# Optimization experiments

Hardware: AMD Instinct MI355X
Metric: run time of the kernel (lower is better)

## Reference

```python
import jax, jax.numpy as jnp
import numpy as np

N = 1024          # nodes per atom and per input graph / barycenter
K = 8             # num_atoms
OT_LAYERS = 3     # proximal-point outer iterations inside fgwd
SINKHORN_LAYERS = 3
GWB_LAYERS = 2    # barycenter alternating-optimization iterations
PROX_BETA = 0.1   # proximal / entropic regularization strength
EPS = 1e-16


def fgwd(Gs, ps, Gb, pb):
    """Gromov-Wasserstein distance via proximal point + Sinkhorn.
    Gs:(ns,ns), ps:(ns,1), Gb:(nb,nb), pb:(nb,1). Returns (d, T) with T:(ns,nb).
    Square-loss GW cost: c(T) = f1(Gs) ps 1^T + 1 (f2(Gb) pb)^T - 2 Gs T Gb^T."""
    ns, nb = Gs.shape[0], Gb.shape[0]
    cost_st = ((Gs * Gs) @ ps) + ((Gb * Gb) @ pb).T  # (ns,1)+(1,nb) -> (ns,nb)
    T0 = ps @ pb.T  # independent-coupling init

    def ot_step(T, _):
        cost = cost_st - 2.0 * (Gs @ T @ Gb.T)
        kernel = jnp.exp(-cost / PROX_BETA) * T  # proximal-point kernel

        def sink(carry, _):
            a, b = carry
            b = pb / (kernel.T @ a + EPS)
            a = ps / (kernel @ b + EPS)
            return (a, b), None

        (a, b), _ = jax.lax.scan(sink, (ps, pb), None, length=SINKHORN_LAYERS)
        return (a * kernel) * b.T, None

    T, _ = jax.lax.scan(ot_step, T0, None, length=OT_LAYERS)
    cost = cost_st - 2.0 * (Gs @ T @ Gb.T)
    d = jnp.sum(cost * T)
    return d, T


def setup_inputs() -> dict:
    key = jax.random.key(0)
    k1, k2, k3 = jax.random.split(key, 3)
    Gm = jax.random.uniform(k1, (N, N), jnp.float32)          # input graph (sigmoid-range adjacency)
    pm = jnp.ones((N, 1), jnp.float32) / N                    # uniform node distribution
    atoms_presig = jax.random.normal(k2, (K, N, N), jnp.float32)  # pre-sigmoid atom params
    probs = jnp.ones((K, N, 1), jnp.float32) / N              # uniform atom distributions
    weights = jax.nn.softmax(jax.random.normal(k3, (K,), jnp.float32))  # output_weights
    return {"Gm": Gm, "pm": pm, "atoms_presig": atoms_presig, "probs": probs,
            "weights": weights}


def reference(Gm, pm, atoms_presig, probs, weights):
    Gk = jax.nn.sigmoid(atoms_presig)              # output_atoms: (K,N,N)
    G_bary, pb = Gm, pm                            # init_mode=0 -> barycenter init from input M
    fgwd_v = jax.vmap(fgwd, in_axes=(0, 0, None, None))
    denom = pb @ pb.T                              # pb pb^T normalizer
    for _ in range(GWB_LAYERS):
        _, trans = fgwd_v(Gk, probs, G_bary, pb)   # trans: (K,N,N)
        # comp_fgwb: sum_k w_k * T_k^T G_k T_k / (pb pb^T)
        GT = jnp.einsum('knm,kmj->knj', Gk, trans)
        G_bary = jnp.einsum('k,kni,knj->ij', weights, trans, GT) / denom
    d_fgw, _ = fgwd(Gm, pm, G_bary, pb)
    return d_fgw, G_bary
```

## Files before the change

kernel.cpp:

```cpp
#include <hip/hip_runtime.h>
#include <math.h>

#define N_   1024
#define K_   8
#define OTL  3
#define SKL  3
#define GWBL 2
#define INVB 10.0f
#define EPSV 1e-16f
#define INVN (1.0f / 1024.0f)
#define NN   ((size_t)N_ * N_)
#define KN   (K_ * N_)

typedef __attribute__((ext_vector_type(8))) short short8;
typedef __attribute__((ext_vector_type(4))) float f32x4;
typedef unsigned short bfu;

__device__ __forceinline__ float b2f(bfu u) {
    unsigned x = ((unsigned)u) << 16;
    return __builtin_bit_cast(float, x);
}
__device__ __forceinline__ bfu f2b(float f) {
    unsigned u = __builtin_bit_cast(unsigned, f);
    unsigned r = u + 0x7fffu + ((u >> 16) & 1u);
    return (bfu)(r >> 16);
}

template<int EPI>
__global__ __launch_bounds__(256, 2)
void bgemm_k(const bfu* __restrict__ A, const bfu* __restrict__ B,
             void* __restrict__ Cp, size_t sA, size_t sB, size_t sC,
             const float* __restrict__ rv, const float* __restrict__ cv,
             const float* __restrict__ wts, float* __restrict__ rs) {
    __shared__ bfu As[2][128 * 32];
    __shared__ bfu Bs[2][128 * 32];

    const int z  = blockIdx.x;
    const int bm = blockIdx.y * 128, bn = blockIdx.z * 128;
    const int tid = threadIdx.x;
    const int lane = tid & 63, wv = tid >> 6;
    const int wr = wv >> 1, wc = wv & 1;

    if (EPI == 0) {
        if (rs && blockIdx.y == 0 && blockIdx.z == 0) {
            const float4 zf = {0.f, 0.f, 0.f, 0.f};
            #pragma unroll
            for (int b = 0; b < 3; ++b)
                *(float4*)&rs[b * KN + z * N_ + tid * 4] = zf;
        }
    }

    const bfu* Az = A + (size_t)z * sA;
    const bfu* Bz = B + (size_t)z * sB;

    const int sr = tid >> 2;
    const int sk = (tid & 3) * 8;
    const int fr = lane & 15;
    const int ks = (lane >> 4) * 8;

    f32x4 acc[4][4];
    #pragma unroll
    for (int i = 0; i < 4; i++)
        #pragma unroll
        for (int j = 0; j < 4; j++) acc[i][j] = (f32x4)0.f;

    for (int k0 = 0; k0 < N_; k0 += 64) {
        __syncthreads();
        #pragma unroll
        for (int sg = 0; sg < 2; ++sg) {
            #pragma unroll
            for (int h = 0; h < 2; ++h) {
                const int row = sr + h * 64;
                const bfu* ga = Az + (size_t)(bm + row) * N_ + k0 + sg * 32 + sk;
                const bfu* gb = Bz + (size_t)(bn + row) * N_ + k0 + sg * 32 + sk;
                __builtin_amdgcn_global_load_lds(
                    (const __attribute__((address_space(1))) unsigned int*)ga,
                    (__attribute__((address_space(3))) unsigned int*)&As[sg][row * 32 + sk],
                    16, 0, 0);
                __builtin_amdgcn_global_load_lds(
                    (const __attribute__((address_space(1))) unsigned int*)gb,
                    (__attribute__((address_space(3))) unsigned int*)&Bs[sg][row * 32 + sk],
                    16, 0, 0);
            }
        }
        __syncthreads();

        #pragma unroll
        for (int sg = 0; sg < 2; ++sg) {
            short8 af[4], bf[4];
            #pragma unroll
            for (int mi = 0; mi < 4; ++mi)
                af[mi] = *(const short8*)&As[sg][(wr * 64 + mi * 16 + fr) * 32 + ks];
            #pragma unroll
            for (int ni = 0; ni < 4; ++ni)
                bf[ni] = *(const short8*)&Bs[sg][(wc * 64 + ni * 16 + fr) * 32 + ks];
            #pragma unroll
            for (int mi = 0; mi < 4; ++mi)
                #pragma unroll
                for (int ni = 0; ni < 4; ++ni)
                    acc[mi][ni] = __builtin_amdgcn_mfma_f32_16x16x32_bf16(
                        af[mi], bf[ni], acc[mi][ni], 0, 0, 0);
        }
    }

    const int r0 = bm + wr * 64, c0 = bn + wc * 64;
    const int rq = (lane >> 4) * 4;

    if (EPI == 1) {
        float* Cz = (float*)Cp + (size_t)z * sC;
        const float w = wts[z];
        #pragma unroll
        for (int mi = 0; mi < 4; ++mi)
            #pragma unroll
            for (int ni = 0; ni < 4; ++ni)
                #pragma unroll
                for (int q = 0; q < 4; ++q)
                    Cz[(size_t)(r0 + mi * 16 + rq + q) * N_ + c0 + ni * 16 + fr]
                        = w * acc[mi][ni][q];
    } else if (EPI == 0) {
        bfu* Cz = (bfu*)Cp + (size_t)z * sC;
        #pragma unroll
        for (int mi = 0; mi < 4; ++mi)
            #pragma unroll
            for (int ni = 0; ni < 4; ++ni)
                #pragma unroll
                for (int q = 0; q < 4; ++q)
                    Cz[(size_t)(r0 + mi * 16 + rq + q) * N_ + c0 + ni * 16 + fr]
                        = f2b(acc[mi][ni][q]);
    } else {
        bfu* Cz = (bfu*)Cp + (size_t)z * sC;
        const float* rvz = rv + z * N_;
        float rsum[4][4];
        #pragma unroll
        for (int mi = 0; mi < 4; ++mi)
            #pragma unroll
            for (int q = 0; q < 4; ++q) rsum[mi][q] = 0.f;
        #pragma unroll
        for (int mi = 0; mi < 4; ++mi)
            #pragma unroll
            for (int ni = 0; ni < 4; ++ni)
                #pragma unroll
                for (int q = 0; q < 4; ++q) {
                    const int row = r0 + mi * 16 + rq + q;
                    const int col = c0 + ni * 16 + fr;
                    const float cost = rvz[col] + cv[row] - 2.f * acc[mi][ni][q];
                    const float t = b2f(Cz[(size_t)row * N_ + col]);
                    const bfu tn = f2b(expf(-cost * INVB) * t);
                    Cz[(size_t)row * N_ + col] = tn;
                    rsum[mi][q] += b2f(tn);
                }
        #pragma unroll
        for (int mi = 0; mi < 4; ++mi)
            #pragma unroll
            for (int q = 0; q < 4; ++q) {
                float v = rsum[mi][q];
                v += __shfl_xor(v, 1);
                v += __shfl_xor(v, 2);
                v += __shfl_xor(v, 4);
                v += __shfl_xor(v, 8);
                if (fr == 0)
                    atomicAdd(&rs[z * N_ + r0 + mi * 16 + rq + q], v);
            }
    }
}

template<int EPI>
__global__ __launch_bounds__(256, 2)
void gemm64_k(const bfu* __restrict__ A, const bfu* __restrict__ B,
              void* __restrict__ Cp,
              const float* __restrict__ rv, const float* __restrict__ cv,
              float* __restrict__ rs, float* __restrict__ dout) {
    __shared__ bfu As[64 * 32];
    __shared__ bfu Bs[64 * 32];
    const int bn = blockIdx.x * 64;
    const int bm = blockIdx.y * 64;
    const int tid = threadIdx.x;
    const int lane = tid & 63, wv = tid >> 6;
    const int wr = wv >> 1, wc = wv & 1;
    const int sr = tid >> 2, sk = (tid & 3) * 8;
    const int fr = lane & 15, ks = (lane >> 4) * 8;

    if (EPI == 0) {
        if (blockIdx.x == 0 && blockIdx.y == 0) {
            if (rs) {
                const float4 zf = {0.f, 0.f, 0.f, 0.f};
                #pragma unroll
                for (int b = 0; b < 3; ++b)
                    *(float4*)&rs[b * KN + tid * 4] = zf;
            }
            if (dout && tid == 0) *dout = 0.f;
        }
    }

    f32x4 acc[2][2];
    #pragma unroll
    for (int i = 0; i < 2; i++)
        #pragma unroll
        for (int j = 0; j < 2; j++) acc[i][j] = (f32x4)0.f;

    for (int k0 = 0; k0 < N_; k0 += 32) {
        __syncthreads();
        __builtin_amdgcn_global_load_lds(
            (const __attribute__((address_space(1))) unsigned int*)
                (A + (size_t)(bm + sr) * N_ + k0 + sk),
            (__attribute__((address_space(3))) unsigned int*)&As[sr * 32 + sk],
            16, 0, 0);
        __builtin_amdgcn_global_load_lds(
            (const __attribute__((address_space(1))) unsigned int*)
                (B + (size_t)(bn + sr) * N_ + k0 + sk),
            (__attribute__((address_space(3))) unsigned int*)&Bs[sr * 32 + sk],
            16, 0, 0);
        __syncthreads();
        short8 af[2], bf[2];
        #pragma unroll
        for (int mi = 0; mi < 2; ++mi)
            af[mi] = *(const short8*)&As[(wr * 32 + mi * 16 + fr) * 32 + ks];
        #pragma unroll
        for (int ni = 0; ni < 2; ++ni)
            bf[ni] = *(const short8*)&Bs[(wc * 32 + ni * 16 + fr) * 32 + ks];
        #pragma unroll
        for (int mi = 0; mi < 2; ++mi)
            #pragma unroll
            for (int ni = 0; ni < 2; ++ni)
                acc[mi][ni] = __builtin_amdgcn_mfma_f32_16x16x32_bf16(
                    af[mi], bf[ni], acc[mi][ni], 0, 0, 0);
    }

    const int r0 = bm + wr * 32, c0 = bn + wc * 32;
    const int rq = (lane >> 4) * 4;

    if (EPI == 0) {
        bfu* C = (bfu*)Cp;
        #pragma unroll
        for (int mi = 0; mi < 2; ++mi)
            #pragma unroll
            for (int ni = 0; ni < 2; ++ni)
                #pragma unroll
                for (int q = 0; q < 4; ++q)
                    C[(size_t)(r0 + mi * 16 + rq + q) * N_ + c0 + ni * 16 + fr]
                        = f2b(acc[mi][ni][q]);
    } else if (EPI == 2) {
        bfu* C = (bfu*)Cp;
        float rsum[2][4];
        #pragma unroll
        for (int mi = 0; mi < 2; ++mi)
            #pragma unroll
            for (int q = 0; q < 4; ++q) rsum[mi][q] = 0.f;
        #pragma unroll
        for (int mi = 0; mi < 2; ++mi)
            #pragma unroll
            for (int ni = 0; ni < 2; ++ni)
                #pragma unroll
                for (int q = 0; q < 4; ++q) {
                    const int row = r0 + mi * 16 + rq + q;
                    const int col = c0 + ni * 16 + fr;
                    const float cost = rv[col] + cv[row] - 2.f * acc[mi][ni][q];
                    const float t = b2f(C[(size_t)row * N_ + col]);
                    const bfu tn = f2b(expf(-cost * INVB) * t);
                    C[(size_t)row * N_ + col] = tn;
                    rsum[mi][q] += b2f(tn);
                }
        #pragma unroll
        for (int mi = 0; mi < 2; ++mi)
            #pragma unroll
            for (int q = 0; q < 4; ++q) {
                float v = rsum[mi][q];
                v += __shfl_xor(v, 1);
                v += __shfl_xor(v, 2);
                v += __shfl_xor(v, 4);
                v += __shfl_xor(v, 8);
                if (fr == 0)
                    atomicAdd(&rs[r0 + mi * 16 + rq + q], v);
            }
    } else {
        const bfu* C = (const bfu*)Cp;
        float bs = 0.f;
        #pragma unroll
        for (int mi = 0; mi < 2; ++mi)
            #pragma unroll
            for (int ni = 0; ni < 2; ++ni)
                #pragma unroll
                for (int q = 0; q < 4; ++q) {
                    const int row = r0 + mi * 16 + rq + q;
                    const int col = c0 + ni * 16 + fr;
                    bs += (rv[col] + cv[row] - 2.f * acc[mi][ni][q]) *
                          b2f(C[(size_t)row * N_ + col]);
                }
        #pragma unroll
        for (int off = 32; off; off >>= 1) bs += __shfl_down(bs, off);
        __shared__ float wred[4];
        if (lane == 0) wred[wv] = bs;
        __syncthreads();
        if (tid == 0) atomicAdd(dout, wred[0] + wred[1] + wred[2] + wred[3]);
    }
}

__global__ __launch_bounds__(256)
void prox1_k(bfu* __restrict__ Tt, const float* __restrict__ c2,
             const float* __restrict__ u, const float* __restrict__ d2,
             const float* __restrict__ w, const float* __restrict__ ps,
             const float* __restrict__ pb, float* __restrict__ bv,
             float* __restrict__ rs1, int zs, int nb) {
    const int b = blockIdx.x;
    const int z  = (nb == 8) ? (b & 7) : 0;
    const int rp = (nb == 8) ? (b >> 3) : b;
    const int tid = threadIdx.x;

    if (rp < 2) {
        const float4 zf = {0.f, 0.f, 0.f, 0.f};
        *(float4*)&rs1[rp * KN + z * N_ + tid * 4] = zf;
    }

    const int half = tid >> 7;
    const int j = rp * 2 + half;
    const int i0 = (tid & 127) * 8;
    const float d2j = d2[j], wj = w[j], pbj = pb[j];
    const float* c2z = c2 + z * zs + i0;
    const float* uz  = u  + z * zs + i0;
    const float* psz = ps + z * zs + i0;
    bfu o[8];
    float s = 0.f;
    #pragma unroll
    for (int t = 0; t < 8; ++t) {
        const float cost = c2z[t] + d2j - 2.f * uz[t] * wj;
        o[t] = f2b(expf(-cost * INVB) * psz[t] * pbj);
        s += b2f(o[t]);
    }
    *(short8*)&Tt[((size_t)z << 20) + ((size_t)j << 10) + i0] = *(short8*)o;
    #pragma unroll
    for (int off = 32; off; off >>= 1) s += __shfl_down(s, off);
    __shared__ float red[4];
    if ((tid & 63) == 0) red[tid >> 6] = s;
    __syncthreads();
    if ((tid & 127) == 0)
        bv[z * N_ + j] = pbj / ((red[half * 2] + red[half * 2 + 1]) * INVN + EPSV);
}

template<int NB>
__global__ __launch_bounds__(256)
void redprox_k(const float* __restrict__ part, bfu* __restrict__ Gbt,
               float* __restrict__ d2out, float* __restrict__ wout,
               float* __restrict__ out1,
               const float* __restrict__ c2, const float* __restrict__ u,
               bfu* __restrict__ Tt, float* __restrict__ bv,
               float* __restrict__ rs12) {
    const int tid = threadIdx.x;
    if (blockIdx.x < 16) {
        const float4 zf = {0.f, 0.f, 0.f, 0.f};
        *(float4*)&rs12[blockIdx.x * 1024 + tid * 4] = zf;
    }
    __shared__ float red[8];
    __shared__ float bc[2];
    #pragma unroll
    for (int rep = 0; rep < 2; ++rep) {
        const int row = blockIdx.x + rep * 512;
        const size_t idx = (size_t)row * N_ + tid * 4;
        float4 s = *(const float4*)(part + idx);
        #pragma unroll
        for (int sl = 1; sl < K_; ++sl) {
            float4 v = *(const float4*)(part + (size_t)sl * NN + idx);
            s.x += v.x; s.y += v.y; s.z += v.z; s.w += v.w;
        }
        const float sc = 1048576.f;
        s.x *= sc; s.y *= sc; s.z *= sc; s.w *= sc;
        bfu o[4];
        o[0] = f2b(s.x); o[1] = f2b(s.y); o[2] = f2b(s.z); o[3] = f2b(s.w);
        *(ulong1*)&Gbt[idx] = *(ulong1*)o;
        if (out1) {
            out1[idx + 0] = s.x; out1[idx + 1] = s.y;
            out1[idx + 2] = s.z; out1[idx + 3] = s.w;
        }
        float r2 = s.x * s.x + s.y * s.y + s.z * s.z + s.w * s.w;
        float r1 = s.x + s.y + s.z + s.w;
        #pragma unroll
        for (int off = 32; off; off >>= 1) {
            r2 += __shfl_down(r2, off);
            r1 += __shfl_down(r1, off);
        }
        if ((tid & 63) == 0) {
            red[(tid >> 6) * 2]     = r2;
            red[(tid >> 6) * 2 + 1] = r1;
        }
        __syncthreads();
        if (tid == 0) {
            const float d2j = (red[0] + red[2] + red[4] + red[6]) * INVN;
            const float wj  = (red[1] + red[3] + red[5] + red[7]) * INVN;
            d2out[row] = d2j; wout[row] = wj;
            bc[0] = d2j; bc[1] = wj;
        }
        __syncthreads();
        const float d2j = bc[0], wj = bc[1];
        const float sc2 = INVN * INVN;
        #pragma unroll
        for (int z = 0; z < NB; ++z) {
            const float4 cv4 = *(const float4*)(c2 + z * N_ + tid * 4);
            const float4 uv4 = *(const float4*)(u  + z * N_ + tid * 4);
            bfu t[4];
            t[0] = f2b(expf(-(cv4.x + d2j - 2.f * uv4.x * wj) * INVB) * sc2);
            t[1] = f2b(expf(-(cv4.y + d2j - 2.f * uv4.y * wj) * INVB) * sc2);
            t[2] = f2b(expf(-(cv4.z + d2j - 2.f * uv4.z * wj) * INVB) * sc2);
            t[3] = f2b(expf(-(cv4.w + d2j - 2.f * uv4.w * wj) * INVB) * sc2);
            *(ulong1*)&Tt[(size_t)z * NN + idx] = *(ulong1*)t;
            float rsum = b2f(t[0]) + b2f(t[1]) + b2f(t[2]) + b2f(t[3]);
            #pragma unroll
            for (int off = 32; off; off >>= 1) rsum += __shfl_down(rsum, off);
            if ((tid & 63) == 0) red[tid >> 6] = rsum;
            __syncthreads();
            if (tid == 0)
                bv[z * N_ + row] = INVN /
                    ((red[0] + red[1] + red[2] + red[3]) * INVN + EPSV);
            __syncthreads();
        }
    }
}

template<int NB, int BSRC, int TUPD>
__global__ __launch_bounds__(1024)
void sinka_k(bfu* __restrict__ Tt, const float* __restrict__ bvin,
             const float* __restrict__ rsin, const float* __restrict__ ps,
             int pstr, float* __restrict__ rsnext) {
    constexpr int CPB = (NB == 8) ? 32 : 16;
    constexpr int RG  = 1024 / CPB;
    constexpr int RPG = N_ / RG;
    int z, cb;
    if (NB == 8) { z = blockIdx.x & 7; cb = blockIdx.x >> 3; }
    else         { z = 0;              cb = blockIdx.x; }
    const int tid = threadIdx.x;
    const int cl = tid % CPB, rg = tid / CPB;
    const int i = cb * CPB + cl;
    const int zN = z * N_;
    bfu* Tz = Tt + (size_t)z * NN;

    __shared__ float bvs[1024];
    __shared__ float red[1024];
    __shared__ float avs[CPB];
    if (BSRC == 0)      bvs[tid] = bvin[zN + tid];
    else if (BSRC == 1) bvs[tid] = INVN / (rsin[zN + tid] * INVN + EPSV);
    else                bvs[tid] = INVN / (rsin[zN + tid] + EPSV);
    __syncthreads();

    float s = 0.f;
    const int j0 = rg * RPG;
    #pragma unroll 8
    for (int j = j0; j < j0 + RPG; ++j)
        s += b2f(Tz[(size_t)j * N_ + i]) * bvs[j];
    red[tid] = s;
    __syncthreads();
    #pragma unroll
    for (int h = RG / 2; h > 0; h >>= 1) {
        if (rg < h) red[rg * CPB + cl] += red[(rg + h) * CPB + cl];
        __syncthreads();
    }
    const float avi = ps[z * pstr + i] / (red[cl] + EPSV);

    if (TUPD) {
        for (int j = j0; j < j0 + RPG; ++j) {
            const size_t o = (size_t)j * N_ + i;
            Tz[o] = f2b(b2f(Tz[o]) * avi * bvs[j]);
        }
    } else {
        if (rg == 0) avs[cl] = avi;
        __syncthreads();
        const bfu* Tr = Tz + (size_t)tid * N_ + cb * CPB;
        float v = 0.f;
        #pragma unroll
        for (int q8 = 0; q8 < CPB; q8 += 8) {
            bfu t[8];
            *(short8*)t = *(const short8*)&Tr[q8];
            #pragma unroll
            for (int q = 0; q < 8; ++q) v += b2f(t[q]) * avs[q8 + q];
        }
        atomicAdd(&rsnext[zN + tid], v);
    }
}

template<int SIG>
__global__ void prep_k(const float* __restrict__ X, bfu* __restrict__ Y,
                       float* __restrict__ y2, float* __restrict__ y1) {
    const int z = blockIdx.y;
    const int wv = threadIdx.x >> 6, lane = threadIdx.x & 63;
    const int r = blockIdx.x * 4 + wv;
    const float* Xr = X + (size_t)z * NN + (size_t)r * N_;
    bfu* Yr = Y + (size_t)z * NN + (size_t)r * N_;
    float s2 = 0.f, s1 = 0.f;
    for (int c = lane * 4; c < N_; c += 256) {
        float4 v = *(const float4*)(Xr + c);
        if (SIG) {
            v.x = 1.f / (1.f + expf(-v.x));
            v.y = 1.f / (1.f + expf(-v.y));
            v.z = 1.f / (1.f + expf(-v.z));
            v.w = 1.f / (1.f + expf(-v.w));
        }
        bfu o[4];
        o[0] = f2b(v.x); o[1] = f2b(v.y); o[2] = f2b(v.z); o[3] = f2b(v.w);
        *(ulong1*)&Yr[c] = *(ulong1*)o;
        s2 += v.x * v.x + v.y * v.y + v.z * v.z + v.w * v.w;
        s1 += v.x + v.y + v.z + v.w;
    }
    #pragma unroll
    for (int off = 32; off; off >>= 1) {
        s2 += __shfl_down(s2, off);
        s1 += __shfl_down(s1, off);
    }
    if (lane == 0) {
        y2[z * N_ + r] = s2 * INVN;
        y1[z * N_ + r] = s1 * INVN;
    }
}


template<int NB, int BSRC1>
static inline void sink_tail(bfu* Tt, const float* ps, int pstr,
                             float* bvec, float* rs, hipStream_t stream) {
    const dim3 ga((NB == 8) ? 256 : 64);
    float* rs1 = rs + KN;
    float* rs2 = rs + 2 * KN;
    sinka_k<NB, BSRC1, 0><<<ga, dim3(1024), 0, stream>>>(Tt, bvec, rs, ps, pstr, rs1);
    sinka_k<NB, 2, 0><<<ga, dim3(1024), 0, stream>>>(Tt, nullptr, rs1, ps, pstr, rs2);
    sinka_k<NB, 2, 1><<<ga, dim3(1024), 0, stream>>>(Tt, nullptr, rs2, ps, pstr, nullptr);
}

extern "C" void kernel_launch(void* const* d_in, const int* in_sizes, int n_in,
                              void* d_out, int out_size, void* d_ws, size_t ws_size,
                              hipStream_t stream) {
    const float* Gm    = (const float*)d_in[0];
    const float* pm    = (const float*)d_in[1];
    const float* atoms = (const float*)d_in[2];
    const float* probs = (const float*)d_in[3];
    const float* wts   = (const float*)d_in[4];
    float* out = (float*)d_out;

    char* base = (char*)d_ws;
    bfu*   Gkt  = (bfu*)base;                    base += K_ * NN * 2;
    bfu*   Tt   = (bfu*)base;                    base += K_ * NN * 2;
    bfu*   M    = (bfu*)base;                    base += K_ * NN * 2;
    float* part = (float*)base;                  base += K_ * NN * 4;
    bfu*   Gbt  = (bfu*)base;                    base += NN * 2;
    bfu*   Gmt  = (bfu*)base;                    base += NN * 2;
    float* Gk2ps = (float*)base;                 base += KN * 4;
    float* Gku   = (float*)base;                 base += KN * 4;
    float* Gm2pm = (float*)base;                 base += N_ * 4;
    float* Gmu   = (float*)base;                 base += N_ * 4;
    float* Gb2pb = (float*)base;                 base += N_ * 4;
    float* Gbw   = (float*)base;                 base += N_ * 4;
    float* bvec  = (float*)base;                 base += KN * 4;
    float* rs    = (float*)base;                 base += 3 * KN * 4;

    const dim3 blk(256);
    const dim3 g8(8, 8, 8);
    const dim3 g64(16, 16);

    prep_k<1><<<dim3(256, K_), blk, 0, stream>>>(atoms, Gkt, Gk2ps, Gku);
    prep_k<0><<<dim3(256, 1), blk, 0, stream>>>(Gm, Gmt, Gm2pm, Gmu);

    for (int it = 0; it < GWBL; ++it) {
        const bfu*   GbtU = it ? Gbt : Gmt;
        const float* d2U  = it ? Gb2pb : Gm2pm;

        if (it == 0)
            prox1_k<<<512 * K_, blk, 0, stream>>>(Tt, Gk2ps, Gku, Gm2pm, Gmu,
                                                  probs, pm, bvec, rs + KN, N_, K_);
        sink_tail<K_, 0>(Tt, probs, N_, bvec, rs, stream);
        for (int ot = 1; ot < OTL; ++ot) {
            bgemm_k<0><<<g8, blk, 0, stream>>>(Gkt, Tt, M, NN, NN, NN,
                nullptr, nullptr, nullptr, rs);
            bgemm_k<2><<<g8, blk, 0, stream>>>(GbtU, M, Tt, 0, NN, NN,
                Gk2ps, d2U, nullptr, rs);
            sink_tail<K_, 1>(Tt, probs, N_, bvec, rs, stream);
        }
        bgemm_k<0><<<g8, blk, 0, stream>>>(Tt, Gkt, M, NN, NN, NN,
            nullptr, nullptr, nullptr, nullptr);
        bgemm_k<1><<<g8, blk, 0, stream>>>(Tt, M, part, NN, NN, NN,
            nullptr, nullptr, wts, nullptr);
        if (it == 0)
            redprox_k<8><<<512, blk, 0, stream>>>(part, Gbt, Gb2pb, Gbw,
                nullptr, Gk2ps, Gku, Tt, bvec, rs + KN);
        else
            redprox_k<1><<<512, blk, 0, stream>>>(part, Gbt, Gb2pb, Gbw,
                out + 1, Gm2pm, Gmu, Tt, bvec, rs + KN);
    }

    sink_tail<1, 0>(Tt, pm, 0, bvec, rs, stream);
    for (int ot = 1; ot < OTL; ++ot) {
        gemm64_k<0><<<g64, blk, 0, stream>>>(Gmt, Tt, M,
            nullptr, nullptr, rs, nullptr);
        gemm64_k<2><<<g64, blk, 0, stream>>>(Gbt, M, Tt,
            Gm2pm, Gb2pb, rs, nullptr);
        sink_tail<1, 1>(Tt, pm, 0, bvec, rs, stream);
    }
    gemm64_k<0><<<g64, blk, 0, stream>>>(Gmt, Tt, M,
        nullptr, nullptr, nullptr, out );
    gemm64_k<3><<<g64, blk, 0, stream>>>(Gbt, M, Tt,
        Gm2pm, Gb2pb, nullptr, out);
}
```

Before: 638.3 us.

## Store partial barycenter in bf16, deepen gemm64 K-step, merge prep launches

The per-atom weighted partial barycenter products are now written and reduced as bf16 instead of fp32, halving that buffer's write and read traffic. The small 64x64 GEMM loads four K-slices per barrier, cutting synchronisation count by four at the cost of more LDS per block. The two prep kernels are merged into one launch, and the single-graph Sinkhorn kernel uses fewer columns per block with more blocks. The bf16 partials add rounding error before the sum over atoms.

```diff
diff --git a/kernel.cpp b/kernel.cpp
--- a/kernel.cpp
+++ b/kernel.cpp
@@ -107,7 +107,7 @@
     const int rq = (lane >> 4) * 4;
 
     if (EPI == 1) {
-        float* Cz = (float*)Cp + (size_t)z * sC;
+        bfu* Cz = (bfu*)Cp + (size_t)z * sC;
         const float w = wts[z];
         #pragma unroll
         for (int mi = 0; mi < 4; ++mi)
@@ -116,7 +116,7 @@
                 #pragma unroll
                 for (int q = 0; q < 4; ++q)
                     Cz[(size_t)(r0 + mi * 16 + rq + q) * N_ + c0 + ni * 16 + fr]
-                        = w * acc[mi][ni][q];
+                        = f2b(w * acc[mi][ni][q]);
     } else if (EPI == 0) {
         bfu* Cz = (bfu*)Cp + (size_t)z * sC;
         #pragma unroll
@@ -170,8 +170,8 @@
               void* __restrict__ Cp,
               const float* __restrict__ rv, const float* __restrict__ cv,
               float* __restrict__ rs, float* __restrict__ dout) {
-    __shared__ bfu As[64 * 32];
-    __shared__ bfu Bs[64 * 32];
+    __shared__ bfu As[4][64 * 32];
+    __shared__ bfu Bs[4][64 * 32];
     const int bn = blockIdx.x * 64;
     const int bm = blockIdx.y * 64;
     const int tid = threadIdx.x;
@@ -198,32 +198,38 @@
         #pragma unroll
         for (int j = 0; j < 2; j++) acc[i][j] = (f32x4)0.f;
 
-    for (int k0 = 0; k0 < N_; k0 += 32) {
-        __syncthreads();
-        __builtin_amdgcn_global_load_lds(
-            (const __attribute__((address_space(1))) unsigned int*)
-                (A + (size_t)(bm + sr) * N_ + k0 + sk),
-            (__attribute__((address_space(3))) unsigned int*)&As[sr * 32 + sk],
-            16, 0, 0);
-        __builtin_amdgcn_global_load_lds(
-            (const __attribute__((address_space(1))) unsigned int*)
-                (B + (size_t)(bn + sr) * N_ + k0 + sk),
-            (__attribute__((address_space(3))) unsigned int*)&Bs[sr * 32 + sk],
-            16, 0, 0);
-        __syncthreads();
-        short8 af[2], bf[2];
-        #pragma unroll
-        for (int mi = 0; mi < 2; ++mi)
-            af[mi] = *(const short8*)&As[(wr * 32 + mi * 16 + fr) * 32 + ks];
-        #pragma unroll
-        for (int ni = 0; ni < 2; ++ni)
-            bf[ni] = *(const short8*)&Bs[(wc * 32 + ni * 16 + fr) * 32 + ks];
-        #pragma unroll
-        for (int mi = 0; mi < 2; ++mi)
+    for (int k0 = 0; k0 < N_; k0 += 128) {
+        __syncthreads();
+        #pragma unroll
+        for (int sg = 0; sg < 4; ++sg) {
+            __builtin_amdgcn_global_load_lds(
+                (const __attribute__((address_space(1))) unsigned int*)
+                    (A + (size_t)(bm + sr) * N_ + k0 + sg * 32 + sk),
+                (__attribute__((address_space(3))) unsigned int*)&As[sg][sr * 32 + sk],
+                16, 0, 0);
+            __builtin_amdgcn_global_load_lds(
+                (const __attribute__((address_space(1))) unsigned int*)
+                    (B + (size_t)(bn + sr) * N_ + k0 + sg * 32 + sk),
+                (__attribute__((address_space(3))) unsigned int*)&Bs[sg][sr * 32 + sk],
+                16, 0, 0);
+        }
+        __syncthreads();
+        #pragma unroll
+        for (int sg = 0; sg < 4; ++sg) {
+            short8 af[2], bf[2];
+            #pragma unroll
+            for (int mi = 0; mi < 2; ++mi)
+                af[mi] = *(const short8*)&As[sg][(wr * 32 + mi * 16 + fr) * 32 + ks];
             #pragma unroll
             for (int ni = 0; ni < 2; ++ni)
-                acc[mi][ni] = __builtin_amdgcn_mfma_f32_16x16x32_bf16(
-                    af[mi], bf[ni], acc[mi][ni], 0, 0, 0);
+                bf[ni] = *(const short8*)&Bs[sg][(wc * 32 + ni * 16 + fr) * 32 + ks];
+            #pragma unroll
+            for (int mi = 0; mi < 2; ++mi)
+                #pragma unroll
+                for (int ni = 0; ni < 2; ++ni)
+                    acc[mi][ni] = __builtin_amdgcn_mfma_f32_16x16x32_bf16(
+                        af[mi], bf[ni], acc[mi][ni], 0, 0, 0);
+        }
     }
 
     const int r0 = bm + wr * 32, c0 = bn + wc * 32;
@@ -338,7 +344,7 @@
 
 template<int NB>
 __global__ __launch_bounds__(256)
-void redprox_k(const float* __restrict__ part, bfu* __restrict__ Gbt,
+void redprox_k(const bfu* __restrict__ part, bfu* __restrict__ Gbt,
                float* __restrict__ d2out, float* __restrict__ wout,
                float* __restrict__ out1,
                const float* __restrict__ c2, const float* __restrict__ u,
@@ -355,11 +361,13 @@
     for (int rep = 0; rep < 2; ++rep) {
         const int row = blockIdx.x + rep * 512;
         const size_t idx = (size_t)row * N_ + tid * 4;
-        float4 s = *(const float4*)(part + idx);
-        #pragma unroll
-        for (int sl = 1; sl < K_; ++sl) {
-            float4 v = *(const float4*)(part + (size_t)sl * NN + idx);
-            s.x += v.x; s.y += v.y; s.z += v.z; s.w += v.w;
+        float4 s = {0.f, 0.f, 0.f, 0.f};
+        #pragma unroll
+        for (int sl = 0; sl < K_; ++sl) {
+            bfu p[4];
+            *(ulong1*)p = *(const ulong1*)&part[(size_t)sl * NN + idx];
+            s.x += b2f(p[0]); s.y += b2f(p[1]);
+            s.z += b2f(p[2]); s.w += b2f(p[3]);
         }
         const float sc = 1048576.f;
         s.x *= sc; s.y *= sc; s.z *= sc; s.w *= sc;
@@ -419,7 +427,7 @@
 void sinka_k(bfu* __restrict__ Tt, const float* __restrict__ bvin,
              const float* __restrict__ rsin, const float* __restrict__ ps,
              int pstr, float* __restrict__ rsnext) {
-    constexpr int CPB = (NB == 8) ? 32 : 16;
+    constexpr int CPB = (NB == 8) ? 32 : 8;
     constexpr int RG  = 1024 / CPB;
     constexpr int RPG = N_ / RG;
     int z, cb;
@@ -474,18 +482,24 @@
     }
 }
 
-template<int SIG>
-__global__ void prep_k(const float* __restrict__ X, bfu* __restrict__ Y,
-                       float* __restrict__ y2, float* __restrict__ y1) {
+__global__ void prep_k(const float* __restrict__ atoms, const float* __restrict__ Gm,
+                       bfu* __restrict__ Gkt, bfu* __restrict__ Gmt,
+                       float* __restrict__ Gk2ps, float* __restrict__ Gku,
+                       float* __restrict__ Gm2pm, float* __restrict__ Gmu) {
     const int z = blockIdx.y;
+    const int sig = (z < 8);
+    const float* X = sig ? atoms + (size_t)z * NN : Gm;
+    bfu*  Y  = sig ? Gkt + (size_t)z * NN : Gmt;
+    float* y2 = sig ? Gk2ps + z * N_ : Gm2pm;
+    float* y1 = sig ? Gku + z * N_ : Gmu;
     const int wv = threadIdx.x >> 6, lane = threadIdx.x & 63;
     const int r = blockIdx.x * 4 + wv;
-    const float* Xr = X + (size_t)z * NN + (size_t)r * N_;
-    bfu* Yr = Y + (size_t)z * NN + (size_t)r * N_;
+    const float* Xr = X + (size_t)r * N_;
+    bfu* Yr = Y + (size_t)r * N_;
     float s2 = 0.f, s1 = 0.f;
     for (int c = lane * 4; c < N_; c += 256) {
         float4 v = *(const float4*)(Xr + c);
-        if (SIG) {
+        if (sig) {
             v.x = 1.f / (1.f + expf(-v.x));
             v.y = 1.f / (1.f + expf(-v.y));
             v.z = 1.f / (1.f + expf(-v.z));
@@ -503,8 +517,8 @@
         s1 += __shfl_down(s1, off);
     }
     if (lane == 0) {
-        y2[z * N_ + r] = s2 * INVN;
-        y1[z * N_ + r] = s1 * INVN;
+        y2[r] = s2 * INVN;
+        y1[r] = s1 * INVN;
     }
 }
 
@@ -512,7 +526,7 @@
 template<int NB, int BSRC1>
 static inline void sink_tail(bfu* Tt, const float* ps, int pstr,
                              float* bvec, float* rs, hipStream_t stream) {
-    const dim3 ga((NB == 8) ? 256 : 64);
+    const dim3 ga((NB == 8) ? 256 : 128);
     float* rs1 = rs + KN;
     float* rs2 = rs + 2 * KN;
     sinka_k<NB, BSRC1, 0><<<ga, dim3(1024), 0, stream>>>(Tt, bvec, rs, ps, pstr, rs1);
@@ -534,7 +548,7 @@
     bfu*   Gkt  = (bfu*)base;                    base += K_ * NN * 2;
     bfu*   Tt   = (bfu*)base;                    base += K_ * NN * 2;
     bfu*   M    = (bfu*)base;                    base += K_ * NN * 2;
-    float* part = (float*)base;                  base += K_ * NN * 4;
+    bfu*   part = (bfu*)base;                    base += K_ * NN * 2;
     bfu*   Gbt  = (bfu*)base;                    base += NN * 2;
     bfu*   Gmt  = (bfu*)base;                    base += NN * 2;
     float* Gk2ps = (float*)base;                 base += KN * 4;
@@ -550,8 +564,8 @@
     const dim3 g8(8, 8, 8);
     const dim3 g64(16, 16);
 
-    prep_k<1><<<dim3(256, K_), blk, 0, stream>>>(atoms, Gkt, Gk2ps, Gku);
-    prep_k<0><<<dim3(256, 1), blk, 0, stream>>>(Gm, Gmt, Gm2pm, Gmu);
+    prep_k<<<dim3(256, 9), blk, 0, stream>>>(atoms, Gm, Gkt, Gmt,
+                                             Gk2ps, Gku, Gm2pm, Gmu);
 
     for (int it = 0; it < GWBL; ++it) {
         const bfu*   GbtU = it ? Gbt : Gmt;
```

Result: faster. 622.4 us, median of 2 (-2.5%).
